# Optimization experiments

Measured on AMD Instinct MI355X. Metric: run time of the kernel, lower is better.

Reference implementation:

```python
import jax, jax.numpy as jnp
import numpy as np

N = 10000       # num_nodes
E = 1000        # num_hyperedges
STEPS = 30      # horizon


def setup_inputs() -> dict:
    key = jax.random.key(0)
    k1, k2 = jax.random.split(key, 2)
    infected0 = jax.random.uniform(k1, (N,)) < 0.01
    x = jnp.stack([(~infected0).astype(jnp.float32),
                   infected0.astype(jnp.float32),
                   jnp.zeros((N,), jnp.float32)], axis=1)
    H = (jax.random.uniform(k2, (STEPS - 1, E, N)) < 0.001).astype(jnp.float32)
    beta = jnp.full((N,), 0.01, jnp.float32)
    gamma = jnp.full((N,), 0.038, jnp.float32)
    return {"x": x, "H": H, "beta": beta, "gamma": gamma, "steps": STEPS}


def _simulate(x, H, beta, gamma):
    n = x.shape[0]
    key0 = jax.random.key(42)

    def step(carry, H_t):
        p_prev, s_prev, key = carry
        key, k1, k2 = jax.random.split(key, 3)
        infected = s_prev[:, 1]
        # hypergraph Laplacian step: H_t.T @ (H_t @ infected)
        new_cases = beta * (H_t.T @ (H_t @ infected))
        new_rec = gamma * infected
        p = jnp.stack([p_prev[:, 0] - new_cases,
                       p_prev[:, 1] + new_cases - new_rec,
                       p_prev[:, 2] + new_rec], axis=1)
        p = jnp.clip(p, 0.0, 1.0)
        # per-node stochastic SIR state transitions (vectorized)
        u1 = jax.random.uniform(k1, (n,))
        u2 = jax.random.uniform(k2, (n,))
        was_S = s_prev[:, 0] == 1
        was_I = s_prev[:, 1] == 1
        s_to_I = was_S & (u1 < p[:, 1])
        i_event = was_I & (u1 < p[:, 2])
        i_to_R = i_event & (u2 < 0.5)
        i_to_S = i_event & ~(u2 < 0.5)
        new_S = (was_S & ~s_to_I) | i_to_S
        new_I = s_to_I | (was_I & ~i_event)
        new_R = (~was_S & ~was_I) | i_to_R
        s = jnp.stack([new_S, new_I, new_R], axis=1).astype(x.dtype)
        return (p, s, key), (p, s)

    (_, _, _), (p_seq, s_seq) = jax.lax.scan(step, (x, x, key0), H)
    pathogen = jnp.concatenate([x[None], p_seq], axis=0)    # (steps, N, 3)
    state = jnp.concatenate([x[None], s_seq], axis=0)       # (steps, N, 3)
    return pathogen, state


def reference(x, H, beta, gamma, steps):
    # steps == H.shape[0] + 1 by construction
    return _simulate(x, H, beta, gamma)
```

## Files before the change

### kernel.cpp

```cpp
#include <hip/hip_runtime.h>
#include <stdint.h>

constexpr int NN = 10000;
constexpr int EE = 1000;
constexpr int TT = 30;
constexpr int TS = TT - 1;
constexpr int ROW = NN * 3;
constexpr int S_OFF = TT * ROW;
constexpr int CAP_E = 48;
constexpr int WPR = CAP_E / 2;
constexpr int PREW = 8;
constexpr int SIMT = 1024;
constexpr int NPT  = 10;
constexpr int NROWS = TS * EE;
constexpr int F4R   = NN / 4;
constexpr int RPB   = 20;
constexpr int PK    = 5;
constexpr int SCANB = NROWS / RPB;
static_assert(EE % RPB == 0 && NROWS % RPB == 0 && RPB % PK == 0, "geometry");

__host__ __device__ inline void tf2x32(uint32_t k0, uint32_t k1,
                                       uint32_t x0, uint32_t x1,
                                       uint32_t &o0, uint32_t &o1) {
  uint32_t ks2 = k0 ^ k1 ^ 0x1BD11BDAu;
  x0 += k0; x1 += k1;
#define TFR(r) do { x0 += x1; x1 = (x1 << (r)) | (x1 >> (32 - (r))); x1 ^= x0; } while (0)
  TFR(13); TFR(15); TFR(26); TFR(6);
  x0 += k1;  x1 += ks2 + 1u;
  TFR(17); TFR(29); TFR(16); TFR(24);
  x0 += ks2; x1 += k0 + 2u;
  TFR(13); TFR(15); TFR(26); TFR(6);
  x0 += k0;  x1 += k1 + 3u;
  TFR(17); TFR(29); TFR(16); TFR(24);
  x0 += k1;  x1 += ks2 + 4u;
  TFR(13); TFR(15); TFR(26); TFR(6);
  x0 += ks2; x1 += k0 + 5u;
#undef TFR
  o0 = x0; o1 = x1;
}

__device__ inline float bits_to_uniform(uint32_t bits) {
  float f = __uint_as_float((bits >> 9) | 0x3F800000u) - 1.0f;
  return f < 0.f ? 0.f : f;
}

struct StepKeys { uint32_t k1a[TS], k1b[TS], k2a[TS], k2b[TS]; };

__device__ inline void bar_lds() {
  asm volatile("s_waitcnt lgkmcnt(0)\n\ts_barrier" ::: "memory");
}

__global__ __launch_bounds__(SIMT)
void k_scan(const float* __restrict__ H,
            int* __restrict__ edge_cnt, uint32_t* __restrict__ edge_words,
            unsigned long long* __restrict__ uv, StepKeys keys) {
  const int tid = threadIdx.x;
  const int bi  = blockIdx.x;

  if (bi >= SCANB) {
    const int t = bi - SCANB;
#pragma unroll
    for (int k = 0; k < NPT; ++k) {
      int n = tid + k * SIMT;
      if (n < NN) {
        uint32_t a, b;
        tf2x32(keys.k1a[t], keys.k1b[t], 0u, (uint32_t)n, a, b);
        uint32_t b1 = __float_as_uint(bits_to_uniform(a ^ b));
        tf2x32(keys.k2a[t], keys.k2b[t], 0u, (uint32_t)n, a, b);
        uint32_t b2 = __float_as_uint(bits_to_uniform(a ^ b));
        uv[(size_t)t * NN + n] = (unsigned long long)b1 | ((unsigned long long)b2 << 32);
      }
    }
    return;
  }

  const int base = bi * RPB;
  const int t    = base / EE;
  const int e0   = base - t * EE;

  __shared__ int      scnt_arr[RPB];
  __shared__ uint16_t lists[RPB][CAP_E];
  if (tid < RPB) scnt_arr[tid] = 0;

  const float4* h0 = reinterpret_cast<const float4*>(H) + (size_t)base * F4R;
  const bool has2 = tid < F4R - 2048;

  float4 b0[PK], b1[PK], b2[PK];
#pragma unroll
  for (int p = 0; p < PK; ++p) {
    const float4* hr = h0 + (size_t)p * F4R;
    b0[p] = hr[tid];
    b1[p] = hr[tid + 1024];
    b2[p] = has2 ? hr[tid + 2048] : make_float4(0.f, 0.f, 0.f, 0.f);
  }
  bar_lds();

#define PROCS(vv, b4, rr) do { \
  if ((vv).x != 0.f) { int q = atomicAdd(&scnt_arr[rr], 1); if (q < CAP_E) lists[rr][q] = (uint16_t)((b4) + 0); } \
  if ((vv).y != 0.f) { int q = atomicAdd(&scnt_arr[rr], 1); if (q < CAP_E) lists[rr][q] = (uint16_t)((b4) + 1); } \
  if ((vv).z != 0.f) { int q = atomicAdd(&scnt_arr[rr], 1); if (q < CAP_E) lists[rr][q] = (uint16_t)((b4) + 2); } \
  if ((vv).w != 0.f) { int q = atomicAdd(&scnt_arr[rr], 1); if (q < CAP_E) lists[rr][q] = (uint16_t)((b4) + 3); } \
} while (0)

  for (int o = 0; o < RPB / PK; ++o) {
#pragma unroll
    for (int p = 0; p < PK; ++p) {
      const int r = o * PK + p;
      float4 va = b0[p], vb = b1[p], vc = b2[p];
      if (o + 1 < RPB / PK) {
        const float4* hr = h0 + (size_t)(r + PK) * F4R;
        b0[p] = hr[tid];
        b1[p] = hr[tid + 1024];
        if (has2) b2[p] = hr[tid + 2048];
      }
      PROCS(va, 4 * tid, r);
      PROCS(vb, 4 * (tid + 1024), r);
      if (has2) PROCS(vc, 4 * (tid + 2048), r);
      bar_lds();
      int c = scnt_arr[r]; c = c < CAP_E ? c : CAP_E;
      const int row = base + r, e = e0 + r;
      if (tid == 0) edge_cnt[row] = c;
      int words = (c + 1) >> 1;
      int wmax = words > PREW ? words : PREW;
      if (tid < wmax) {
        uint32_t lo = (2 * tid     < c) ? (uint32_t)lists[r][2 * tid]     : 0xFFFFu;
        uint32_t hi = (2 * tid + 1 < c) ? (uint32_t)lists[r][2 * tid + 1] : 0xFFFFu;
        edge_words[((size_t)t * WPR + tid) * EE + e] = lo | (hi << 16);
      }
    }
  }
#undef PROCS
}

__global__ __launch_bounds__(SIMT, 4)
void k_sim(const int* __restrict__ edge_cnt, const uint32_t* __restrict__ edge_words,
           const unsigned long long* __restrict__ uv,
           const float* __restrict__ x,
           const float* __restrict__ beta, const float* __restrict__ gamma_,
           float* __restrict__ out) {
  const int tid = threadIdx.x;
  __shared__ int nvst[NN];
  __shared__ unsigned char st8[NN];

  float p0a[NPT], p1a[NPT], p2a[NPT], bet[NPT], gam[NPT];
#pragma unroll
  for (int k = 0; k < NPT; ++k) {
    int n = tid + k * SIMT;
    if (n < NN) {
      float x0 = x[n * 3 + 0], x1 = x[n * 3 + 1], x2 = x[n * 3 + 2];
      p0a[k] = x0; p1a[k] = x1; p2a[k] = x2;
      st8[n] = (unsigned char)((x1 == 1.f) ? 1 : ((x0 == 1.f) ? 0 : 2));
      nvst[n] = 0;
      bet[k] = beta[n]; gam[k] = gamma_[n];
      out[n * 3 + 0] = x0; out[n * 3 + 1] = x1; out[n * 3 + 2] = x2;
      out[S_OFF + n * 3 + 0] = x0; out[S_OFF + n * 3 + 1] = x1; out[S_OFF + n * 3 + 2] = x2;
    }
  }

  int ec = 0; uint32_t w[PREW];
  float u1r[NPT], u2r[NPT];
  if (tid < EE) {
    ec = edge_cnt[tid]; if (ec > CAP_E) ec = CAP_E;
#pragma unroll
    for (int j = 0; j < PREW; ++j) w[j] = edge_words[((size_t)0 * WPR + j) * EE + tid];
  }
#pragma unroll
  for (int k = 0; k < NPT; ++k) {
    int n = tid + k * SIMT;
    if (n < NN) {
      unsigned long long raw = uv[n];
      u1r[k] = __uint_as_float((uint32_t)raw);
      u2r[k] = __uint_as_float((uint32_t)(raw >> 32));
    }
  }
  bar_lds();

  for (int t = 0; t < TS; ++t) {
    if (tid < EE) {
      const uint32_t* wb = edge_words + (size_t)t * WPR * EE + tid;
      int words = (ec + 1) >> 1;
      int s = 0;
#pragma unroll
      for (int j = 0; j < PREW; ++j) {
        uint32_t lo = w[j] & 0xFFFFu, hi = w[j] >> 16;
        if (lo != 0xFFFFu) s += (st8[lo] == 1) ? 1 : 0;
        if (hi != 0xFFFFu) s += (st8[hi] == 1) ? 1 : 0;
      }
      for (int j = PREW; j < words; ++j) {
        uint32_t ww = wb[(size_t)j * EE];
        uint32_t lo = ww & 0xFFFFu, hi = ww >> 16;
        if (lo != 0xFFFFu) s += (st8[lo] == 1) ? 1 : 0;
        if (hi != 0xFFFFu) s += (st8[hi] == 1) ? 1 : 0;
      }
      if (s > 0) {
#pragma unroll
        for (int j = 0; j < PREW; ++j) {
          uint32_t lo = w[j] & 0xFFFFu, hi = w[j] >> 16;
          if (lo != 0xFFFFu) atomicAdd(&nvst[lo], s);
          if (hi != 0xFFFFu) atomicAdd(&nvst[hi], s);
        }
        for (int j = PREW; j < words; ++j) {
          uint32_t ww = wb[(size_t)j * EE];
          uint32_t lo = ww & 0xFFFFu, hi = ww >> 16;
          if (lo != 0xFFFFu) atomicAdd(&nvst[lo], s);
          if (hi != 0xFFFFu) atomicAdd(&nvst[hi], s);
        }
      }
    }
    bar_lds();

    int ecn = 0; uint32_t wn[PREW];
    {
      const int tn = (t + 1 < TS) ? t + 1 : t;
      if (tid < EE) {
        ecn = edge_cnt[tn * EE + tid]; if (ecn > CAP_E) ecn = CAP_E;
#pragma unroll
        for (int j = 0; j < PREW; ++j) wn[j] = edge_words[((size_t)tn * WPR + j) * EE + tid];
      }
    }

    float* po = out + (size_t)(t + 1) * ROW;
    float* so = out + S_OFF + (size_t)(t + 1) * ROW;
#pragma unroll
    for (int k = 0; k < NPT; ++k) {
      int n = tid + k * SIMT;
      if (n < NN) {
        int v  = nvst[n];
        int st = (int)st8[n];
        float s1 = (st == 1) ? 1.f : 0.f;
        float new_cases = __fmul_rn(bet[k], (float)v);
        float new_rec   = __fmul_rn(gam[k], s1);
        float q0 = fminf(1.f, fmaxf(0.f, __fsub_rn(p0a[k], new_cases)));
        float q1 = fminf(1.f, fmaxf(0.f, __fsub_rn(__fadd_rn(p1a[k], new_cases), new_rec)));
        float q2 = fminf(1.f, fmaxf(0.f, __fadd_rn(p2a[k], new_rec)));
        p0a[k] = q0; p1a[k] = q1; p2a[k] = q2;

        bool was_S  = (st == 0);
        bool was_I  = (st == 1);
        bool s_to_I = was_S && (u1r[k] < q1);
        bool i_event = was_I && (u1r[k] < q2);
        bool u2lt   = (u2r[k] < 0.5f);
        bool i_to_R = i_event && u2lt;
        bool i_to_S = i_event && !u2lt;
        bool new_S = (was_S && !s_to_I) || i_to_S;
        bool new_I = s_to_I || (was_I && !i_event);
        bool new_R = (!was_S && !was_I) || i_to_R;

        po[n * 3 + 0] = q0; po[n * 3 + 1] = q1; po[n * 3 + 2] = q2;
        so[n * 3 + 0] = new_S ? 1.f : 0.f;
        so[n * 3 + 1] = new_I ? 1.f : 0.f;
        so[n * 3 + 2] = new_R ? 1.f : 0.f;
        st8[n] = (unsigned char)(new_I ? 1 : (new_S ? 0 : 2));
        nvst[n] = 0;
      }
    }

    if (t + 1 < TS) {
#pragma unroll
      for (int k = 0; k < NPT; ++k) {
        int n = tid + k * SIMT;
        if (n < NN) {
          unsigned long long raw = uv[(size_t)(t + 1) * NN + n];
          u1r[k] = __uint_as_float((uint32_t)raw);
          u2r[k] = __uint_as_float((uint32_t)(raw >> 32));
        }
      }
    }
    bar_lds();

    ec = ecn;
#pragma unroll
    for (int j = 0; j < PREW; ++j) w[j] = wn[j];
  }
}

extern "C" void kernel_launch(void* const* d_in, const int* in_sizes, int n_in,
                              void* d_out, int out_size, void* d_ws, size_t ws_size,
                              hipStream_t stream) {
  const float* x      = (const float*)d_in[0];
  const float* H      = (const float*)d_in[1];
  const float* beta   = (const float*)d_in[2];
  const float* gamma_ = (const float*)d_in[3];
  float* out = (float*)d_out;

  StepKeys keys;
  uint32_t key0 = 0u, key1 = 42u;
  for (int t = 0; t < TS; ++t) {
    uint32_t a0, b0, a1, b1, a2, b2;
    tf2x32(key0, key1, 0u, 0u, a0, b0);
    tf2x32(key0, key1, 0u, 1u, a1, b1);
    tf2x32(key0, key1, 0u, 2u, a2, b2);
    keys.k1a[t] = a1; keys.k1b[t] = b1; keys.k2a[t] = a2; keys.k2b[t] = b2;
    key0 = a0; key1 = b0;
  }

  size_t off = 0;
  auto take = [&](size_t bytes) { size_t o = off; off += (bytes + 255) & ~(size_t)255; return o; };
  size_t o_ec = take((size_t)NROWS * sizeof(int));
  size_t o_ew = take((size_t)TS * WPR * EE * sizeof(uint32_t));
  size_t o_uv = take((size_t)TS * NN * sizeof(unsigned long long));

  int*      edge_cnt   = (int*)((char*)d_ws + o_ec);
  uint32_t* edge_words = (uint32_t*)((char*)d_ws + o_ew);
  unsigned long long* uvp = (unsigned long long*)((char*)d_ws + o_uv);

  k_scan<<<SCANB + TS, SIMT, 0, stream>>>(H, edge_cnt, edge_words, uvp, keys);
  k_sim<<<1, SIMT, 0, stream>>>(edge_cnt, edge_words, uvp, x, beta, gamma_, out);
}
```

Baseline: 1.696 ms.

## Fuse scan and simulation kernels with per-step global counters for overlap

Merges the H-scanning/RNG kernel and the single-block simulation kernel into one launch. Block 0 runs the simulation and spins on per-timestep global counters until that step's edge lists and random numbers are ready. This lets step t run while later timesteps of H are still being scanned. The cost is a co-residency dependence, since block 0 must be scheduled early, which holds because it has the lowest block index. Loads and stores of the shared intermediates become relaxed agent-scope atomics, and an extra zeroing kernel is launched.

```diff
diff --git a/kernel.cpp b/kernel.cpp
--- a/kernel.cpp
+++ b/kernel.cpp
@@ -17,6 +17,7 @@
 constexpr int RPB   = 20;
 constexpr int PK    = 5;
 constexpr int SCANB = NROWS / RPB;
+constexpr unsigned GATE = EE + 1;
 static_assert(EE % RPB == 0 && NROWS % RPB == 0 && RPB % PK == 0, "geometry");
 
 __host__ __device__ inline void tf2x32(uint32_t k0, uint32_t k1,
@@ -50,15 +51,25 @@
   asm volatile("s_waitcnt lgkmcnt(0)\n\ts_barrier" ::: "memory");
 }
 
-__global__ __launch_bounds__(SIMT)
-void k_scan(const float* __restrict__ H,
-            int* __restrict__ edge_cnt, uint32_t* __restrict__ edge_words,
-            unsigned long long* __restrict__ uv, StepKeys keys) {
+#define ALD(p)     __hip_atomic_load((p),  __ATOMIC_RELAXED, __HIP_MEMORY_SCOPE_AGENT)
+#define AST(p, v)  __hip_atomic_store((p), (v), __ATOMIC_RELAXED, __HIP_MEMORY_SCOPE_AGENT)
+
+__global__ void k_zero(unsigned* __restrict__ cnt) {
+  if (threadIdx.x < TS) cnt[threadIdx.x] = 0u;
+}
+
+__global__ __launch_bounds__(SIMT, 4)
+void k_fused(const float* __restrict__ H,
+             int* __restrict__ edge_cnt, uint32_t* __restrict__ edge_words,
+             unsigned long long* __restrict__ uv, unsigned* __restrict__ cntg,
+             const float* __restrict__ x,
+             const float* __restrict__ beta, const float* __restrict__ gamma_,
+             float* __restrict__ out, StepKeys keys) {
   const int tid = threadIdx.x;
   const int bi  = blockIdx.x;
 
-  if (bi >= SCANB) {
-    const int t = bi - SCANB;
+  if (bi >= 1 && bi <= TS) {
+    const int t = bi - 1;
 #pragma unroll
     for (int k = 0; k < NPT; ++k) {
       int n = tid + k * SIMT;
@@ -68,81 +79,84 @@
         uint32_t b1 = __float_as_uint(bits_to_uniform(a ^ b));
         tf2x32(keys.k2a[t], keys.k2b[t], 0u, (uint32_t)n, a, b);
         uint32_t b2 = __float_as_uint(bits_to_uniform(a ^ b));
-        uv[(size_t)t * NN + n] = (unsigned long long)b1 | ((unsigned long long)b2 << 32);
-      }
-    }
+        unsigned long long raw = (unsigned long long)b1 | ((unsigned long long)b2 << 32);
+        AST(&uv[(size_t)t * NN + n], raw);
+      }
+    }
+    __syncthreads();
+    if (tid == 0)
+      __hip_atomic_fetch_add(&cntg[t], 1u, __ATOMIC_RELAXED, __HIP_MEMORY_SCOPE_AGENT);
     return;
   }
 
-  const int base = bi * RPB;
-  const int t    = base / EE;
-  const int e0   = base - t * EE;
-
-  __shared__ int      scnt_arr[RPB];
-  __shared__ uint16_t lists[RPB][CAP_E];
-  if (tid < RPB) scnt_arr[tid] = 0;
-
-  const float4* h0 = reinterpret_cast<const float4*>(H) + (size_t)base * F4R;
-  const bool has2 = tid < F4R - 2048;
-
-  float4 b0[PK], b1[PK], b2[PK];
-#pragma unroll
-  for (int p = 0; p < PK; ++p) {
-    const float4* hr = h0 + (size_t)p * F4R;
-    b0[p] = hr[tid];
-    b1[p] = hr[tid + 1024];
-    b2[p] = has2 ? hr[tid + 2048] : make_float4(0.f, 0.f, 0.f, 0.f);
-  }
-  bar_lds();
+  if (bi > TS) {
+    const int base = (bi - 1 - TS) * RPB;
+    const int t    = base / EE;
+    const int e0   = base - t * EE;
+
+    __shared__ int      scnt_arr[RPB];
+    __shared__ uint16_t lists[RPB][CAP_E];
+    if (tid < RPB) scnt_arr[tid] = 0;
+
+    const float4* h0 = reinterpret_cast<const float4*>(H) + (size_t)base * F4R;
+    const bool has2 = tid < F4R - 2048;
+
+    float4 b0[PK], b1[PK], b2[PK];
+#pragma unroll
+    for (int p = 0; p < PK; ++p) {
+      const float4* hr = h0 + (size_t)p * F4R;
+      b0[p] = hr[tid];
+      b1[p] = hr[tid + 1024];
+      b2[p] = has2 ? hr[tid + 2048] : make_float4(0.f, 0.f, 0.f, 0.f);
+    }
+    bar_lds();
 
 #define PROCS(vv, b4, rr) do { \
-  if ((vv).x != 0.f) { int q = atomicAdd(&scnt_arr[rr], 1); if (q < CAP_E) lists[rr][q] = (uint16_t)((b4) + 0); } \
-  if ((vv).y != 0.f) { int q = atomicAdd(&scnt_arr[rr], 1); if (q < CAP_E) lists[rr][q] = (uint16_t)((b4) + 1); } \
-  if ((vv).z != 0.f) { int q = atomicAdd(&scnt_arr[rr], 1); if (q < CAP_E) lists[rr][q] = (uint16_t)((b4) + 2); } \
-  if ((vv).w != 0.f) { int q = atomicAdd(&scnt_arr[rr], 1); if (q < CAP_E) lists[rr][q] = (uint16_t)((b4) + 3); } \
-} while (0)
-
-  for (int o = 0; o < RPB / PK; ++o) {
-#pragma unroll
-    for (int p = 0; p < PK; ++p) {
-      const int r = o * PK + p;
-      float4 va = b0[p], vb = b1[p], vc = b2[p];
-      if (o + 1 < RPB / PK) {
-        const float4* hr = h0 + (size_t)(r + PK) * F4R;
-        b0[p] = hr[tid];
-        b1[p] = hr[tid + 1024];
-        if (has2) b2[p] = hr[tid + 2048];
-      }
-      PROCS(va, 4 * tid, r);
-      PROCS(vb, 4 * (tid + 1024), r);
-      if (has2) PROCS(vc, 4 * (tid + 2048), r);
-      bar_lds();
-      int c = scnt_arr[r]; c = c < CAP_E ? c : CAP_E;
-      const int row = base + r, e = e0 + r;
-      if (tid == 0) edge_cnt[row] = c;
-      int words = (c + 1) >> 1;
-      int wmax = words > PREW ? words : PREW;
-      if (tid < wmax) {
-        uint32_t lo = (2 * tid     < c) ? (uint32_t)lists[r][2 * tid]     : 0xFFFFu;
-        uint32_t hi = (2 * tid + 1 < c) ? (uint32_t)lists[r][2 * tid + 1] : 0xFFFFu;
-        edge_words[((size_t)t * WPR + tid) * EE + e] = lo | (hi << 16);
-      }
-    }
-  }
+    if ((vv).x != 0.f) { int q = atomicAdd(&scnt_arr[rr], 1); if (q < CAP_E) lists[rr][q] = (uint16_t)((b4) + 0); } \
+    if ((vv).y != 0.f) { int q = atomicAdd(&scnt_arr[rr], 1); if (q < CAP_E) lists[rr][q] = (uint16_t)((b4) + 1); } \
+    if ((vv).z != 0.f) { int q = atomicAdd(&scnt_arr[rr], 1); if (q < CAP_E) lists[rr][q] = (uint16_t)((b4) + 2); } \
+    if ((vv).w != 0.f) { int q = atomicAdd(&scnt_arr[rr], 1); if (q < CAP_E) lists[rr][q] = (uint16_t)((b4) + 3); } \
+  } while (0)
+
+    for (int o = 0; o < RPB / PK; ++o) {
+#pragma unroll
+      for (int p = 0; p < PK; ++p) {
+        const int r = o * PK + p;
+        float4 va = b0[p], vb = b1[p], vc = b2[p];
+        if (o + 1 < RPB / PK) {
+          const float4* hr = h0 + (size_t)(r + PK) * F4R;
+          b0[p] = hr[tid];
+          b1[p] = hr[tid + 1024];
+          if (has2) b2[p] = hr[tid + 2048];
+        }
+        PROCS(va, 4 * tid, r);
+        PROCS(vb, 4 * (tid + 1024), r);
+        if (has2) PROCS(vc, 4 * (tid + 2048), r);
+        bar_lds();
+        int c = scnt_arr[r]; c = c < CAP_E ? c : CAP_E;
+        const int row = base + r, e = e0 + r;
+        if (tid == 0) AST(&edge_cnt[row], c);
+        int words = (c + 1) >> 1;
+        int wmax = words > PREW ? words : PREW;
+        if (tid < wmax) {
+          uint32_t lo = (2 * tid     < c) ? (uint32_t)lists[r][2 * tid]     : 0xFFFFu;
+          uint32_t hi = (2 * tid + 1 < c) ? (uint32_t)lists[r][2 * tid + 1] : 0xFFFFu;
+          AST(&edge_words[((size_t)t * WPR + tid) * EE + e], lo | (hi << 16));
+        }
+      }
+    }
 #undef PROCS
-}
-
-__global__ __launch_bounds__(SIMT, 4)
-void k_sim(const int* __restrict__ edge_cnt, const uint32_t* __restrict__ edge_words,
-           const unsigned long long* __restrict__ uv,
-           const float* __restrict__ x,
-           const float* __restrict__ beta, const float* __restrict__ gamma_,
-           float* __restrict__ out) {
-  const int tid = threadIdx.x;
+    __syncthreads();
+    if (tid == 0)
+      __hip_atomic_fetch_add(&cntg[t], (unsigned)RPB,
+                             __ATOMIC_RELAXED, __HIP_MEMORY_SCOPE_AGENT);
+    return;
+  }
+
   __shared__ int nvst[NN];
   __shared__ unsigned char st8[NN];
 
-  float p0a[NPT], p1a[NPT], p2a[NPT], bet[NPT], gam[NPT];
+  float p0a[NPT], p1a[NPT], p2a[NPT], bet[NPT], gam[NPT], u1r[NPT], u2r[NPT];
 #pragma unroll
   for (int k = 0; k < NPT; ++k) {
     int n = tid + k * SIMT;
@@ -156,24 +170,27 @@
       out[S_OFF + n * 3 + 0] = x0; out[S_OFF + n * 3 + 1] = x1; out[S_OFF + n * 3 + 2] = x2;
     }
   }
-
+  bar_lds();
+
+  if (tid == 0) {
+    while (ALD(&cntg[0]) < GATE) __builtin_amdgcn_s_sleep(1);
+  }
+  bar_lds();
   int ec = 0; uint32_t w[PREW];
-  float u1r[NPT], u2r[NPT];
   if (tid < EE) {
-    ec = edge_cnt[tid]; if (ec > CAP_E) ec = CAP_E;
-#pragma unroll
-    for (int j = 0; j < PREW; ++j) w[j] = edge_words[((size_t)0 * WPR + j) * EE + tid];
+    ec = ALD(&edge_cnt[tid]); if (ec > CAP_E) ec = CAP_E;
+#pragma unroll
+    for (int j = 0; j < PREW; ++j) w[j] = ALD(&edge_words[(size_t)j * EE + tid]);
   }
 #pragma unroll
   for (int k = 0; k < NPT; ++k) {
     int n = tid + k * SIMT;
     if (n < NN) {
-      unsigned long long raw = uv[n];
+      unsigned long long raw = ALD(&uv[n]);
       u1r[k] = __uint_as_float((uint32_t)raw);
       u2r[k] = __uint_as_float((uint32_t)(raw >> 32));
     }
   }
-  bar_lds();
 
   for (int t = 0; t < TS; ++t) {
     if (tid < EE) {
@@ -187,7 +204,7 @@
         if (hi != 0xFFFFu) s += (st8[hi] == 1) ? 1 : 0;
       }
       for (int j = PREW; j < words; ++j) {
-        uint32_t ww = wb[(size_t)j * EE];
+        uint32_t ww = ALD(&wb[(size_t)j * EE]);
         uint32_t lo = ww & 0xFFFFu, hi = ww >> 16;
         if (lo != 0xFFFFu) s += (st8[lo] == 1) ? 1 : 0;
         if (hi != 0xFFFFu) s += (st8[hi] == 1) ? 1 : 0;
@@ -200,7 +217,7 @@
           if (hi != 0xFFFFu) atomicAdd(&nvst[hi], s);
         }
         for (int j = PREW; j < words; ++j) {
-          uint32_t ww = wb[(size_t)j * EE];
+          uint32_t ww = ALD(&wb[(size_t)j * EE]);
           uint32_t lo = ww & 0xFFFFu, hi = ww >> 16;
           if (lo != 0xFFFFu) atomicAdd(&nvst[lo], s);
           if (hi != 0xFFFFu) atomicAdd(&nvst[hi], s);
@@ -209,14 +226,17 @@
     }
     bar_lds();
 
+    const bool more = (t + 1 < TS);
+    if (more && tid == 0) {
+      while (ALD(&cntg[t + 1]) < GATE) __builtin_amdgcn_s_sleep(1);
+    }
+    bar_lds();
     int ecn = 0; uint32_t wn[PREW];
-    {
-      const int tn = (t + 1 < TS) ? t + 1 : t;
-      if (tid < EE) {
-        ecn = edge_cnt[tn * EE + tid]; if (ecn > CAP_E) ecn = CAP_E;
-#pragma unroll
-        for (int j = 0; j < PREW; ++j) wn[j] = edge_words[((size_t)tn * WPR + j) * EE + tid];
-      }
+    if (more && tid < EE) {
+      ecn = ALD(&edge_cnt[(t + 1) * EE + tid]); if (ecn > CAP_E) ecn = CAP_E;
+#pragma unroll
+      for (int j = 0; j < PREW; ++j)
+        wn[j] = ALD(&edge_words[((size_t)(t + 1) * WPR + j) * EE + tid]);
     }
 
     float* po = out + (size_t)(t + 1) * ROW;
@@ -255,22 +275,21 @@
       }
     }
 
-    if (t + 1 < TS) {
+    if (more) {
 #pragma unroll
       for (int k = 0; k < NPT; ++k) {
         int n = tid + k * SIMT;
         if (n < NN) {
-          unsigned long long raw = uv[(size_t)(t + 1) * NN + n];
+          unsigned long long raw = ALD(&uv[(size_t)(t + 1) * NN + n]);
           u1r[k] = __uint_as_float((uint32_t)raw);
           u2r[k] = __uint_as_float((uint32_t)(raw >> 32));
         }
       }
+      ec = ecn;
+#pragma unroll
+      for (int j = 0; j < PREW; ++j) w[j] = wn[j];
     }
     bar_lds();
-
-    ec = ecn;
-#pragma unroll
-    for (int j = 0; j < PREW; ++j) w[j] = wn[j];
   }
 }
 
@@ -299,11 +318,14 @@
   size_t o_ec = take((size_t)NROWS * sizeof(int));
   size_t o_ew = take((size_t)TS * WPR * EE * sizeof(uint32_t));
   size_t o_uv = take((size_t)TS * NN * sizeof(unsigned long long));
+  size_t o_ct = take((size_t)TS * sizeof(unsigned));
 
   int*      edge_cnt   = (int*)((char*)d_ws + o_ec);
   uint32_t* edge_words = (uint32_t*)((char*)d_ws + o_ew);
   unsigned long long* uvp = (unsigned long long*)((char*)d_ws + o_uv);
-
-  k_scan<<<SCANB + TS, SIMT, 0, stream>>>(H, edge_cnt, edge_words, uvp, keys);
-  k_sim<<<1, SIMT, 0, stream>>>(edge_cnt, edge_words, uvp, x, beta, gamma_, out);
-}
+  unsigned* cnt        = (unsigned*)((char*)d_ws + o_ct);
+
+  k_zero<<<1, 64, 0, stream>>>(cnt);
+  k_fused<<<1 + TS + SCANB, SIMT, 0, stream>>>(H, edge_cnt, edge_words, uvp, cnt,
+                                               x, beta, gamma_, out, keys);
+}
```

New measurement: 1.693 ms. Within noise of the previous version (-0.2%).
